# Performance work log

Measured on AMD Instinct MI355X. Metric: run time of the kernel, lower is better.

Reference implementation:

```python
import jax, jax.numpy as jnp
import numpy as np

MAX_SEQ_LEN = 4096
N_QUBITS = 11
N_LAYERS = 2
DIM = 2 ** N_QUBITS


def setup_inputs() -> dict:
    key = jax.random.key(0)
    k_theta, = jax.random.split(key, 1)
    # matches nn.Parameter(torch.randn(max_seq_len, n_layers, 3*n_qubits) * 0.1)
    theta = jax.random.normal(k_theta, (MAX_SEQ_LEN, N_LAYERS, 3 * N_QUBITS), dtype=jnp.float32) * 0.1
    positions = jnp.arange(MAX_SEQ_LEN, dtype=jnp.int32)
    return {"theta": theta, "positions": positions}


def _gate_matrices(theta_sel):
    """theta_sel: (B, L, 3Q) -> combined single-qubit unitaries U = Rz @ Ry @ Rx, (B, L, Q, 2, 2) complex64."""
    B = theta_sel.shape[0]
    ang = theta_sel.reshape(B, N_LAYERS, N_QUBITS, 3) * 0.5  # half angles
    a, b, g = ang[..., 0], ang[..., 1], ang[..., 2]  # rx, ry, rz
    ca, sa = jnp.cos(a), jnp.sin(a)
    cb, sb = jnp.cos(b), jnp.sin(b)
    zero = jnp.zeros_like(a) + 0j
    # RX(t) = [[cos t/2, -i sin t/2], [-i sin t/2, cos t/2]]
    Rx = jnp.stack([jnp.stack([ca + 0j, -1j * sa], -1),
                    jnp.stack([-1j * sa, ca + 0j], -1)], -2)
    # RY(t) = [[cos, -sin], [sin, cos]]
    Ry = jnp.stack([jnp.stack([cb + 0j, -sb + 0j], -1),
                    jnp.stack([sb + 0j, cb + 0j], -1)], -2)
    # RZ(t) = diag(e^{-it/2}, e^{+it/2})
    Rz = jnp.stack([jnp.stack([jnp.exp(-1j * g), zero], -1),
                    jnp.stack([zero, jnp.exp(1j * g)], -1)], -2)
    return jnp.einsum('...ij,...jk,...kl->...il', Rz, Ry, Rx).astype(jnp.complex64)


def _simulate(theta_sel):
    """Batched little-endian statevector simulation of the PQC. Returns (B, 2^Q) float32 (real part)."""
    B = theta_sel.shape[0]
    U = _gate_matrices(theta_sel)  # (B, L, Q, 2, 2)
    state = jnp.zeros((B, DIM), jnp.complex64).at[:, 0].set(1.0)  # |0...0>
    for l in range(N_LAYERS):
        # single-qubit RX.RY.RZ block (fused per qubit)
        for q in range(N_QUBITS):
            # qubit q has stride 2^q in little-endian index
            st = state.reshape(B, 2 ** (N_QUBITS - 1 - q), 2, 2 ** q)
            state = jnp.einsum('bij,bhjl->bhil', U[:, l, q], st).reshape(B, DIM)
        # CX ladder: cx(q, q+1) -> control bit q, target bit q+1
        for q in range(N_QUBITS - 1):
            st = state.reshape(B, 2 ** (N_QUBITS - 2 - q), 2, 2, 2 ** q)  # (B, rest, target, control, low)
            c0 = st[:, :, :, 0, :]
            c1 = st[:, :, ::-1, 1, :]  # flip target when control = 1
            state = jnp.stack([c0, c1], axis=3).reshape(B, DIM)
    return state.real.astype(jnp.float32)


def reference(theta, positions):
    return _simulate(theta[positions])
```

## Files before the change

kernel.cpp:

```cpp
#include <hip/hip_runtime.h>
#include <math.h>

#define N_QUBITS 11
#define N_LAYERS 2
#define DIM 2048
#define N_GATES 22
#define ROW 36

typedef float v2f __attribute__((ext_vector_type(2)));
static __device__ __forceinline__ v2f splat(float s) { return (v2f){s, s}; }


static __device__ __forceinline__
void apply5(v2f (&SR)[16], v2f (&SI)[16], const float (*G)[8], int gbase)
{
    {
        const float* g = G[gbase];
        const v2f C0r = {g[0], g[4]}, C0i = {g[1], g[5]};
        const v2f C1r = {g[2], g[6]}, C1i = {g[3], g[7]};
        #pragma unroll
        for (int k = 0; k < 16; ++k) {
            const v2f rx = splat(SR[k].x), ry = splat(SR[k].y);
            const v2f ix = splat(SI[k].x), iy = splat(SI[k].y);
            SR[k] = C0r * rx - C0i * ix + C1r * ry - C1i * iy;
            SI[k] = C0r * ix + C0i * rx + C1r * iy + C1i * ry;
        }
    }
    #pragma unroll
    for (int t = 1; t < 5; ++t) {
        const float* g = G[gbase + t];
        const v2f u00r = splat(g[0]), u00i = splat(g[1]);
        const v2f u01r = splat(g[2]), u01i = splat(g[3]);
        const v2f u10r = splat(g[4]), u10i = splat(g[5]);
        const v2f u11r = splat(g[6]), u11i = splat(g[7]);
        const int h = 1 << (t - 1);
        #pragma unroll
        for (int s = 0; s < 8; ++s) {
            const int k0 = ((s >> (t - 1)) << t) | (s & (h - 1));
            const int k1 = k0 + h;
            const v2f ar = SR[k0], ai = SI[k0];
            const v2f br = SR[k1], bi = SI[k1];
            SR[k0] = u00r * ar - u00i * ai + u01r * br - u01i * bi;
            SI[k0] = u00r * ai + u00i * ar + u01r * bi + u01i * br;
            SR[k1] = u10r * ar - u10i * ai + u11r * br - u11i * bi;
            SI[k1] = u10r * ai + u10i * ar + u11r * bi + u11i * br;
        }
    }
}

static __device__ __forceinline__
void lane_gate_q10(v2f (&SR)[16], v2f (&SI)[16], const float* g, int L)
{
    const int bit = (L >> 5) & 1;
    const v2f csr = splat(bit ? g[6] : g[0]), csi = splat(bit ? g[7] : g[1]);
    const v2f cpr = splat(bit ? g[4] : g[2]), cpi = splat(bit ? g[5] : g[3]);
    #pragma unroll
    for (int k = 0; k < 16; ++k) {
        const double dr = __builtin_bit_cast(double, SR[k]);
        const double di = __builtin_bit_cast(double, SI[k]);
        const v2f pr = __builtin_bit_cast(v2f, __shfl_xor(dr, 32));
        const v2f pi = __builtin_bit_cast(v2f, __shfl_xor(di, 32));
        const v2f ar = SR[k], ai = SI[k];
        SR[k] = csr * ar - csi * ai + cpr * pr - cpi * pi;
        SI[k] = csr * ai + csi * ar + cpr * pi + cpi * pr;
    }
}

static __device__ __forceinline__
void write_rows(float* buf, const v2f (&S)[16], int L)
{
    #pragma unroll
    for (int k = 0; k < 8; ++k) {
        *(float4*)&buf[L * ROW + 4 * k] =
            make_float4(S[2*k].x, S[2*k].y, S[2*k+1].x, S[2*k+1].y);
    }
}

static __device__ __forceinline__
void read_swap(const float* buf, v2f (&S)[16], int L)
{
    const int rb = L & 32;
    const int rr = L & 31;
    #pragma unroll
    for (int t = 0; t < 16; ++t) {
        const float a0 = buf[(2*t     | rb) * ROW + rr];
        const float a1 = buf[((2*t+1) | rb) * ROW + rr];
        S[t] = (v2f){a0, a1};
    }
}

static __device__ __forceinline__
void read_cnot(const float* buf, v2f (&S)[16], int L)
{
    const int gl      = (L ^ (L << 1)) & 31;
    const int lane_or = ((((L >> 5) ^ (L >> 4)) & 1) << 5);
    #pragma unroll
    for (int t = 0; t < 16; ++t) {
        const int n0 = 2 * t, n1 = 2 * t + 1;
        const int f0 = (n0 ^ (n0 << 1)) & 31;
        const int f1 = (n1 ^ (n1 << 1)) & 31;
        const int reg = gl ^ (n0 >> 4);
        const float a0 = buf[(f0 | lane_or) * ROW + reg];
        const float a1 = buf[(f1 | lane_or) * ROW + reg];
        S[t] = (v2f){a0, a1};
    }
}

__global__ __launch_bounds__(64) __attribute__((amdgpu_waves_per_eu(4, 4)))
void pqc_sim_kernel(const float* __restrict__ theta,
                    const int* __restrict__ positions,
                    float* __restrict__ out)
{
    __shared__ float G[N_GATES][8];
    __shared__ float buf[64 * ROW];

    const int b   = blockIdx.x;
    const int L   = threadIdx.x;
    const int pos = positions[b];

    if (L < N_GATES) {
        const int l = L / N_QUBITS;
        const int q = L % N_QUBITS;
        const float* th = theta + (((size_t)pos * N_LAYERS + l) * (3 * N_QUBITS)) + 3 * q;
        const float a  = th[0] * 0.5f;
        const float bb = th[1] * 0.5f;
        const float g  = th[2] * 0.5f;
        float sa, ca, sb, cb, sg, cg;
        sincosf(a,  &sa, &ca);
        sincosf(bb, &sb, &cb);
        sincosf(g,  &sg, &cg);
        const float m00r =  cb * ca, m00i =  sb * sa;
        const float m01r = -sb * ca, m01i = -cb * sa;
        const float m10r =  sb * ca, m10i = -cb * sa;
        const float m11r =  cb * ca, m11i = -sb * sa;
        G[L][0] = m00r * cg + m00i * sg;  G[L][1] = m00i * cg - m00r * sg;
        G[L][2] = m01r * cg + m01i * sg;  G[L][3] = m01i * cg - m01r * sg;
        G[L][4] = m10r * cg - m10i * sg;  G[L][5] = m10i * cg + m10r * sg;
        G[L][6] = m11r * cg - m11i * sg;  G[L][7] = m11i * cg + m11r * sg;
    }
    __syncthreads();

    v2f SR[16], SI[16];
    #pragma unroll
    for (int k = 0; k < 16; ++k) { SR[k] = (v2f){0.f, 0.f}; SI[k] = (v2f){0.f, 0.f}; }

    {
        const int m = L & 31;
        float cr = G[0][(m & 1) ? 4 : 0];
        float ci = G[0][(m & 1) ? 5 : 1];
        #pragma unroll
        for (int q = 1; q < 5; ++q) {
            const int bq = (m >> q) & 1;
            const float gr = G[q][bq ? 4 : 0];
            const float gi = G[q][bq ? 5 : 1];
            const float tr = cr * gr - ci * gi;
            ci = cr * gi + ci * gr;
            cr = tr;
        }
        if (L & 32) { cr = 0.f; ci = 0.f; }
        SR[0].x = cr;
        SI[0].x = ci;
    }
    apply5(SR, SI, G, 5);
    lane_gate_q10(SR, SI, G[10], L);
    write_rows(buf, SR, L);  read_cnot(buf, SR, L);
    write_rows(buf, SI, L);  read_cnot(buf, SI, L);

    apply5(SR, SI, G, 11);
    write_rows(buf, SR, L);  read_swap(buf, SR, L);
    write_rows(buf, SI, L);  read_swap(buf, SI, L);
    apply5(SR, SI, G, 16);
    lane_gate_q10(SR, SI, G[21], L);
    write_rows(buf, SR, L);  read_cnot(buf, SR, L);
    write_rows(buf, SI, L);  read_cnot(buf, SI, L);

    float* orow = out + (size_t)b * DIM + L * 32;
    #pragma unroll
    for (int k = 0; k < 8; ++k) {
        *(float4*)(orow + 4 * k) =
            make_float4(SR[2*k].x, SR[2*k].y, SR[2*k+1].x, SR[2*k+1].y);
    }
}

extern "C" void kernel_launch(void* const* d_in, const int* in_sizes, int n_in,
                              void* d_out, int out_size, void* d_ws, size_t ws_size,
                              hipStream_t stream)
{
    const float* theta     = (const float*)d_in[0];
    const int*   positions = (const int*)d_in[1];
    float*       out       = (float*)d_out;
    const int B = in_sizes[1];

    pqc_sim_kernel<<<B, 64, 0, stream>>>(theta, positions, out);
}
```

Baseline: 90.51 us.

## Build first layer analytically as product state, skipping layer-one gates and CNOT shuffles

```diff
diff --git a/kernel.cpp b/kernel.cpp
--- a/kernel.cpp
+++ b/kernel.cpp
@@ -11,13 +11,28 @@
 static __device__ __forceinline__ v2f splat(float s) { return (v2f){s, s}; }
 
 
+static __device__ __forceinline__ int nofm(int m) {
+    int n = 0, p = 0;
+    #pragma unroll
+    for (int q = 0; q < 5; ++q) { p ^= (m >> q) & 1; n |= p << q; }
+    return n;
+}
+
+static __device__ __forceinline__ float getS(const v2f (&S)[16], int n) {
+    return (n & 1) ? S[n >> 1].y : S[n >> 1].x;
+}
+static __device__ __forceinline__ void setS(v2f (&S)[16], int n, float v) {
+    if (n & 1) S[n >> 1].y = v; else S[n >> 1].x = v;
+}
+
 static __device__ __forceinline__
 void apply5(v2f (&SR)[16], v2f (&SI)[16], const float (*G)[8], int gbase)
 {
     {
-        const float* g = G[gbase];
-        const v2f C0r = {g[0], g[4]}, C0i = {g[1], g[5]};
-        const v2f C1r = {g[2], g[6]}, C1i = {g[3], g[7]};
+        const float4 gA = *(const float4*)&G[gbase][0];
+        const float4 gB = *(const float4*)&G[gbase][4];
+        const v2f C0r = {gA.x, gB.x}, C0i = {gA.y, gB.y};
+        const v2f C1r = {gA.z, gB.z}, C1i = {gA.w, gB.w};
         #pragma unroll
         for (int k = 0; k < 16; ++k) {
             const v2f rx = splat(SR[k].x), ry = splat(SR[k].y);
@@ -28,11 +43,12 @@
     }
     #pragma unroll
     for (int t = 1; t < 5; ++t) {
-        const float* g = G[gbase + t];
-        const v2f u00r = splat(g[0]), u00i = splat(g[1]);
-        const v2f u01r = splat(g[2]), u01i = splat(g[3]);
-        const v2f u10r = splat(g[4]), u10i = splat(g[5]);
-        const v2f u11r = splat(g[6]), u11i = splat(g[7]);
+        const float4 gA = *(const float4*)&G[gbase + t][0];
+        const float4 gB = *(const float4*)&G[gbase + t][4];
+        const v2f u00r = splat(gA.x), u00i = splat(gA.y);
+        const v2f u01r = splat(gA.z), u01i = splat(gA.w);
+        const v2f u10r = splat(gB.x), u10i = splat(gB.y);
+        const v2f u11r = splat(gB.z), u11i = splat(gB.w);
         const int h = 1 << (t - 1);
         #pragma unroll
         for (int s = 0; s < 8; ++s) {
@@ -141,30 +157,63 @@
     __syncthreads();
 
     v2f SR[16], SI[16];
-    #pragma unroll
-    for (int k = 0; k < 16; ++k) { SR[k] = (v2f){0.f, 0.f}; SI[k] = (v2f){0.f, 0.f}; }
 
     {
-        const int m = L & 31;
-        float cr = G[0][(m & 1) ? 4 : 0];
-        float ci = G[0][(m & 1) ? 5 : 1];
+        float car0[5], cai0[5], car1[5], cai1[5];
+        #pragma unroll
+        for (int q = 0; q < 5; ++q) {
+            car0[q] = G[q][0]; cai0[q] = G[q][1];
+            car1[q] = G[q][4]; cai1[q] = G[q][5];
+        }
+        setS(SR, nofm(0), car0[0]);  setS(SI, nofm(0), cai0[0]);
+        setS(SR, nofm(1), car1[0]);  setS(SI, nofm(1), cai1[0]);
         #pragma unroll
         for (int q = 1; q < 5; ++q) {
-            const int bq = (m >> q) & 1;
-            const float gr = G[q][bq ? 4 : 0];
-            const float gi = G[q][bq ? 5 : 1];
-            const float tr = cr * gr - ci * gi;
-            ci = cr * gi + ci * gr;
-            cr = tr;
-        }
-        if (L & 32) { cr = 0.f; ci = 0.f; }
-        SR[0].x = cr;
-        SI[0].x = ci;
-    }
-    apply5(SR, SI, G, 5);
-    lane_gate_q10(SR, SI, G[10], L);
-    write_rows(buf, SR, L);  read_cnot(buf, SR, L);
-    write_rows(buf, SI, L);  read_cnot(buf, SI, L);
+            #pragma unroll
+            for (int m = 0; m < (1 << q); ++m) {
+                const int ns = nofm(m);
+                const int nd = nofm(m | (1 << q));
+                const float ar = getS(SR, ns), ai = getS(SI, ns);
+                setS(SR, nd, ar * car1[q] - ai * cai1[q]);
+                setS(SI, nd, ar * cai1[q] + ai * car1[q]);
+                setS(SR, ns, ar * car0[q] - ai * cai0[q]);
+                setS(SI, ns, ar * cai0[q] + ai * car0[q]);
+            }
+        }
+
+        const int x = L ^ (L >> 1);
+        float plr, pli;
+        {
+            const int bq = x & 1;
+            plr = bq ? G[6][4] : G[6][0];
+            pli = bq ? G[6][5] : G[6][1];
+        }
+        #pragma unroll
+        for (int k = 1; k < 5; ++k) {
+            const int bq = (x >> k) & 1;
+            const float cr = bq ? G[6 + k][4] : G[6 + k][0];
+            const float ci = bq ? G[6 + k][5] : G[6 + k][1];
+            const float tr = plr * cr - pli * ci;
+            pli = plr * ci + pli * cr;
+            plr = tr;
+        }
+        const int l0 = L & 1;
+        const float c5ar = l0 ? G[5][4] : G[5][0];
+        const float c5ai = l0 ? G[5][5] : G[5][1];
+        const float c5br = l0 ? G[5][0] : G[5][4];
+        const float c5bi = l0 ? G[5][1] : G[5][5];
+        const float F0r = plr * c5ar - pli * c5ai, F0i = plr * c5ai + pli * c5ar;
+        const float F1r = plr * c5br - pli * c5bi, F1i = plr * c5bi + pli * c5br;
+
+        #pragma unroll
+        for (int n = 0; n < 32; ++n) {
+            const float fr = (n & 16) ? F1r : F0r;
+            const float fi = (n & 16) ? F1i : F0i;
+            const float ar = getS(SR, n), ai = getS(SI, n);
+            setS(SR, n, ar * fr - ai * fi);
+            setS(SI, n, ar * fi + ai * fr);
+        }
+    }
 
     apply5(SR, SI, G, 11);
     write_rows(buf, SR, L);  read_swap(buf, SR, L);
@@ -172,7 +221,6 @@
     apply5(SR, SI, G, 16);
     lane_gate_q10(SR, SI, G[21], L);
     write_rows(buf, SR, L);  read_cnot(buf, SR, L);
-    write_rows(buf, SI, L);  read_cnot(buf, SI, L);
 
     float* orow = out + (size_t)b * DIM + L * 32;
     #pragma unroll
```

Result: no change. 89.95 us (-0.6%).
